# Kernel tuning notes

Measured on AMD Instinct MI355X. Metric: run time of the kernel, lower is better.

Reference implementation:

```python
import jax, jax.numpy as jnp
import numpy as np

N_LAYERS = 2

def setup_inputs() -> dict:
    key = jax.random.key(0)
    ks = jax.random.split(key, 11)
    B, T, S, H, V = 32, 64, 128, 1024, 32000
    dec_input = jax.random.randint(ks[0], (B, T), 0, V)
    h0 = jax.random.normal(ks[1], (N_LAYERS, B, H), jnp.float32)
    c0 = jax.random.normal(ks[2], (N_LAYERS, B, H), jnp.float32)
    encoder_outputs = jax.random.normal(ks[3], (B, S, H), jnp.float32)
    emb = jax.random.normal(ks[4], (V, H), jnp.float32) * 0.02
    emb = emb.at[0].set(0.0)  # padding_idx = 0
    W_ih = jax.random.normal(ks[5], (N_LAYERS, 4 * H, H), jnp.float32) * 0.02
    W_hh = jax.random.normal(ks[6], (N_LAYERS, 4 * H, H), jnp.float32) * 0.02
    b_ih = jax.random.normal(ks[7], (N_LAYERS, 4 * H), jnp.float32) * 0.02
    b_hh = jax.random.normal(ks[8], (N_LAYERS, 4 * H), jnp.float32) * 0.02
    cls_W = jax.random.normal(ks[9], (V, H), jnp.float32) * 0.02
    cls_b = jax.random.normal(ks[10], (V,), jnp.float32) * 0.02
    return dict(dec_input=dec_input, h0=h0, c0=c0, encoder_outputs=encoder_outputs,
                emb=emb, W_ih=W_ih, W_hh=W_hh, b_ih=b_ih, b_hh=b_hh,
                cls_W=cls_W, cls_b=cls_b)


def reference(dec_input, h0, c0, encoder_outputs, emb, W_ih, W_hh, b_ih, b_hh, cls_W, cls_b):
    # embedding (+dropout p=0) then relu, as in the torch forward
    x = jax.nn.relu(jnp.take(emb, dec_input, axis=0))  # [B,T,H]

    def step(carry, x_t):  # x_t: [B,H]
        h, c = carry  # each [L,B,H]
        inp = x_t
        new_h, new_c = [], []
        for i in range(N_LAYERS):
            gates = inp @ W_ih[i].T + b_ih[i] + h[i] @ W_hh[i].T + b_hh[i]  # [B,4H]
            ig, fg, gg, og = jnp.split(gates, 4, axis=-1)  # PyTorch LSTMCell gate order
            ci = jax.nn.sigmoid(fg) * c[i] + jax.nn.sigmoid(ig) * jnp.tanh(gg)
            hi = jax.nn.sigmoid(og) * jnp.tanh(ci)
            new_h.append(hi)
            new_c.append(ci)
            # residual (dims match since embedding_dim == rnn_dim)
            inp = hi + inp
        last = inp  # StackLSTMCell returns residual-accumulated output
        # dot attention: scores = context bmm target -> softmax (combine Linear output is discarded upstream)
        attn = jax.nn.softmax(jnp.einsum('bsh,bh->bs', encoder_outputs, last), axis=-1)
        return (jnp.stack(new_h), jnp.stack(new_c)), (last, attn)

    (hT, cT), (outs, attns) = jax.lax.scan(step, (h0, c0), jnp.swapaxes(x, 0, 1))
    outputs = jnp.swapaxes(outs, 0, 1)  # [B,T,H]
    logits = jnp.einsum('bth,vh->btv', outputs, cls_W) + cls_b  # [B,T,V]
    attn_scores = jnp.transpose(attns, (1, 2, 0))  # stack dim=2 -> [B,S,T]
    return logits, hT, cT, attn_scores
```

## Files before the change

### kernel.cpp

```cpp
#include <hip/hip_runtime.h>
#include <math.h>

typedef _Float16 f16x8 __attribute__((ext_vector_type(8)));
typedef _Float16 f16x4 __attribute__((ext_vector_type(4)));
typedef float    f32x4 __attribute__((ext_vector_type(4)));
typedef unsigned long long u64;
typedef unsigned int u32;

#define ALOAD(p)    __hip_atomic_load((p), __ATOMIC_RELAXED, __HIP_MEMORY_SCOPE_AGENT)
#define ASTORE(p,v) __hip_atomic_store((p), (v), __ATOMIC_RELAXED, __HIP_MEMORY_SCOPE_AGENT)

__global__ __launch_bounds__(256) void k_f32_to_f16(const float* __restrict__ src,
                                                    _Float16* __restrict__ dst, int n4) {
  int i = blockIdx.x * 256 + threadIdx.x;
  int stride = gridDim.x * 256;
  for (; i < n4; i += stride) {
    float4 v = ((const float4*)src)[i];
    f16x4 o;
    o.x = (_Float16)v.x; o.y = (_Float16)v.y; o.z = (_Float16)v.z; o.w = (_Float16)v.w;
    ((f16x4*)dst)[i] = o;
  }
}

__global__ __launch_bounds__(256) void k_pack0(const float* __restrict__ Whh0,
                                               _Float16* __restrict__ P) {
  int li = blockIdx.x * 256 + threadIdx.x;
  int row = li >> 7, k8 = li & 127;
  const float* s = Whh0 + (size_t)row * 1024 + k8 * 8;
  int g = row >> 10, u = row & 1023, jb = u >> 4, col = u & 15;
  int kh = k8 >> 4, rem = k8 & 15, st = rem >> 2, kslot = rem & 3;
  size_t idx = ((size_t)(((jb * 8 + kh) * 4 + st) * 4 + g)) * 64 + kslot * 16 + col;
  f16x8 o;
#pragma unroll
  for (int j = 0; j < 8; ++j) o[j] = (_Float16)s[j];
  *(f16x8*)(P + idx * 8) = o;
}

__global__ __launch_bounds__(256) void k_pack1(const float* __restrict__ Wih1,
                                               const float* __restrict__ Whh1,
                                               _Float16* __restrict__ P) {
  int li = blockIdx.x * 256 + threadIdx.x;
  int mat = li >> 19;
  int li2 = li & 524287;
  int row = li2 >> 7, k8l = li2 & 127;
  const float* s = (mat ? Whh1 : Wih1) + (size_t)row * 1024 + k8l * 8;
  int g = row >> 10, u = row & 1023, jb = u >> 4, col = u & 15;
  int k8g = mat * 128 + k8l;
  int kh = k8g >> 5, rem = k8g & 31, st = rem >> 2, kslot = rem & 3;
  size_t idx = ((size_t)(((jb * 8 + kh) * 8 + st) * 4 + g)) * 64 + kslot * 16 + col;
  f16x8 o;
#pragma unroll
  for (int j = 0; j < 8; ++j) o[j] = (_Float16)s[j];
  *(f16x8*)(P + idx * 8) = o;
}

__global__ __launch_bounds__(256) void k_embed(const int* __restrict__ dec,
                                               const float* __restrict__ emb,
                                               float* __restrict__ xf,
                                               _Float16* __restrict__ xh) {
  int i = blockIdx.x * 256 + threadIdx.x;
  int r = i >> 8;
  int c4 = i & 255;
  int b = r & 31, t = r >> 5;
  int tok = dec[b * 64 + t];
  float4 v = ((const float4*)(emb + (size_t)tok * 1024))[c4];
  v.x = fmaxf(v.x, 0.f); v.y = fmaxf(v.y, 0.f); v.z = fmaxf(v.z, 0.f); v.w = fmaxf(v.w, 0.f);
  ((float4*)(xf + (size_t)r * 1024))[c4] = v;
  f16x4 o;
  o.x = (_Float16)v.x; o.y = (_Float16)v.y; o.z = (_Float16)v.z; o.w = (_Float16)v.w;
  ((f16x4*)(xh + (size_t)r * 1024))[c4] = o;
}

__global__ __launch_bounds__(256) void k_init(const float* __restrict__ h0, const float* __restrict__ c0,
                                              float* __restrict__ c,
                                              _Float16* __restrict__ h0S, _Float16* __restrict__ h1S,
                                              int* __restrict__ bar) {
  int i = blockIdx.x * 256 + threadIdx.x;
  float hv = h0[i];
  c[i] = c0[i];
  if (i < 32768) h0S[i] = (_Float16)hv;
  else           h1S[i - 32768] = (_Float16)hv;
  if (i < 640) bar[i] = 0;
}

__global__ __launch_bounds__(256) void k_gemm0(const _Float16* __restrict__ A,
                                               const _Float16* __restrict__ Bm,
                                               const float* __restrict__ bias0,
                                               const float* __restrict__ bias1,
                                               float* __restrict__ C) {
  __shared__ _Float16 As[4 * 128 * 8];
  __shared__ _Float16 Bs[4 * 128 * 8];
  const int tid = threadIdx.x;
  const int lane = tid & 63;
  const int w = tid >> 6;
  const int wm = w >> 1, wn = w & 1;
  const _Float16* Ab = A + (size_t)blockIdx.y * 128 * 1024;
  const _Float16* Bb = Bm + (size_t)blockIdx.x * 128 * 1024;
  f32x4 acc[4][4] = {};
  for (int kc = 0; kc < 32; ++kc) {
#pragma unroll
    for (int ii = 0; ii < 2; ++ii) {
      int idx = tid + ii * 256;
      int kb = idx >> 7, row = idx & 127;
      int gofs = row * 1024 + kc * 32 + kb * 8;
      int sofs = kb * 1024 + row * 8;
      *(f16x8*)(As + sofs) = *(const f16x8*)(Ab + gofs);
      *(f16x8*)(Bs + sofs) = *(const f16x8*)(Bb + gofs);
    }
    __syncthreads();
    const int kb = lane >> 4;
    f16x8 af[4], bfv[4];
#pragma unroll
    for (int mf = 0; mf < 4; ++mf) {
      int row = wm * 64 + mf * 16 + (lane & 15);
      af[mf] = *(const f16x8*)(As + kb * 1024 + row * 8);
    }
#pragma unroll
    for (int nf = 0; nf < 4; ++nf) {
      int row = wn * 64 + nf * 16 + (lane & 15);
      bfv[nf] = *(const f16x8*)(Bs + kb * 1024 + row * 8);
    }
#pragma unroll
    for (int mf = 0; mf < 4; ++mf)
#pragma unroll
      for (int nf = 0; nf < 4; ++nf)
        acc[mf][nf] = __builtin_amdgcn_mfma_f32_16x16x32_f16(af[mf], bfv[nf], acc[mf][nf], 0, 0, 0);
    __syncthreads();
  }
  const int rl = (lane >> 4) * 4;
#pragma unroll
  for (int mf = 0; mf < 4; ++mf) {
#pragma unroll
    for (int nf = 0; nf < 4; ++nf) {
#pragma unroll
      for (int j = 0; j < 4; ++j) {
        int m = wm * 64 + mf * 16 + rl + j;
        int n = wn * 64 + nf * 16 + (lane & 15);
        int rg = blockIdx.y * 128 + m;
        int ng = blockIdx.x * 128 + n;
        C[(size_t)rg * 8192 + ng] = acc[mf][nf][j] + bias0[ng] + bias1[ng];
      }
    }
  }
}

__device__ __forceinline__ void gbar(int* bar) {
  __syncthreads();
  if (threadIdx.x == 0) {
    int* gen = bar + 544;
    int g = ALOAD(gen);
    int grp = blockIdx.x >> 3;
    int a = __hip_atomic_fetch_add(bar + grp * 32, 1, __ATOMIC_RELAXED, __HIP_MEMORY_SCOPE_AGENT);
    if (a == 7) {
      ASTORE(bar + grp * 32, 0);
      int r = __hip_atomic_fetch_add(bar + 512, 1, __ATOMIC_RELAXED, __HIP_MEMORY_SCOPE_AGENT);
      if (r == 15) {
        ASTORE(bar + 512, 0);
        ASTORE(gen, g + 1);
      }
    }
    while (ALOAD(gen) == g) __builtin_amdgcn_s_sleep(1);
  }
  __syncthreads();
}

template <int ROLE>
__device__ __forceinline__ void run_phases(
    int jb, const _Float16* __restrict__ Pk,
    const float* __restrict__ gx, const float* __restrict__ x_f,
    float* __restrict__ c_f,
    _Float16* __restrict__ h0S, _Float16* __restrict__ h1S,
    float* __restrict__ ipfA, float* __restrict__ ipfB,
    float* __restrict__ outs_f, _Float16* __restrict__ outs_h,
    float* __restrict__ outHT, float* __restrict__ outCT,
    int* bar, _Float16* As) {
  constexpr int S = ROLE ? 8 : 4;
  constexpr int NHALF = ROLE ? 2 : 1;
  constexpr int RSH = ROLE ? 8 : 7;
  constexpr int K8M = ROLE ? 255 : 127;
  const int u0 = jb * 16;
  const int tid = threadIdx.x;
  const int lane = tid & 63;
  const int kh = tid >> 6;
  const int col = lane & 15;
  const int kslot = lane >> 4;

  float* cst = c_f + ROLE * 32768;
  const float* gxbase = gx + (ROLE ? 4096 : 0);
  const int cb = tid >> 4, cul = tid & 15, cu = u0 + cul;

  const _Float16* pkbase = Pk + ((size_t)(jb * 8 + kh) * S) * 4 * 512 + lane * 8;
  const int a0off = col * 2056 + kh * S * 32 + kslot * 8;
  const int a1off = a0off + 16 * 2056;

  f16x8 wreg[S * 4];
#pragma unroll
  for (int i = 0; i < S * 4; ++i) wreg[i] = *(const f16x8*)(pkbase + i * 512);

  for (int p = 0; p <= 64; ++p) {
    const bool active = (ROLE == 0) ? (p < 64) : (p > 0);
    if (active) {
      const int t = (ROLE == 0) ? p : p - 1;
      const _Float16* h0r = h0S + (size_t)p * 32768;
      _Float16* h0w = h0S + (size_t)(p + 1) * 32768;
      const _Float16* h1r = h1S + (size_t)(p - 1) * 32768;
      _Float16* h1w = h1S + (size_t)p * 32768;
      const float* ipfr; float* ipfw;
      if (p & 1) { ipfr = ipfA; ipfw = ipfB; }
      else       { ipfr = ipfB; ipfw = ipfA; }

      const float* gxr = gxbase + (size_t)(t * 32 + cb) * 8192;
      float pg0 = gxr[cu], pg1 = gxr[1024 + cu], pg2 = gxr[2048 + cu], pg3 = gxr[3072 + cu];
      float pc = cst[cb * 1024 + cu];
      float px = 0.f, pip = 0.f;
      if (ROLE == 0) px = x_f[(size_t)(t * 32 + cb) * 1024 + cu];
      else           pip = ALOAD(ipfr + cb * 1024 + cu);

#pragma unroll
      for (int hf = 0; hf < NHALF; ++hf) {
        f16x8 sreg[8];
#pragma unroll
        for (int i = 0; i < 8; ++i) {
          int fr = (hf * 8 + i) * 512 + tid;
          int row = fr >> RSH, k8 = fr & K8M;
          const _Float16* s;
          if (ROLE == 0) s = h0r + row * 1024 + k8 * 8;
          else           s = (k8 < 128) ? (h0r + row * 1024 + k8 * 8)
                                        : (h1r + row * 1024 + (k8 - 128) * 8);
          sreg[i] = *(const f16x8*)s;
        }
#pragma unroll
        for (int i = 0; i < 8; ++i) {
          int fr = (hf * 8 + i) * 512 + tid;
          int row = fr >> RSH, k8 = fr & K8M;
          *(f16x8*)(As + row * 2056 + k8 * 8) = sreg[i];
        }
      }
      __syncthreads();

      f32x4 acc[2][4] = {};
#pragma unroll
      for (int s2 = 0; s2 < S; ++s2) {
        f16x8 a0 = *(const f16x8*)(As + a0off + s2 * 32);
        f16x8 a1 = *(const f16x8*)(As + a1off + s2 * 32);
        acc[0][0] = __builtin_amdgcn_mfma_f32_16x16x32_f16(a0, wreg[s2 * 4 + 0], acc[0][0], 0, 0, 0);
        acc[1][0] = __builtin_amdgcn_mfma_f32_16x16x32_f16(a1, wreg[s2 * 4 + 0], acc[1][0], 0, 0, 0);
        acc[0][1] = __builtin_amdgcn_mfma_f32_16x16x32_f16(a0, wreg[s2 * 4 + 1], acc[0][1], 0, 0, 0);
        acc[1][1] = __builtin_amdgcn_mfma_f32_16x16x32_f16(a1, wreg[s2 * 4 + 1], acc[1][1], 0, 0, 0);
        acc[0][2] = __builtin_amdgcn_mfma_f32_16x16x32_f16(a0, wreg[s2 * 4 + 2], acc[0][2], 0, 0, 0);
        acc[1][2] = __builtin_amdgcn_mfma_f32_16x16x32_f16(a1, wreg[s2 * 4 + 2], acc[1][2], 0, 0, 0);
        acc[0][3] = __builtin_amdgcn_mfma_f32_16x16x32_f16(a0, wreg[s2 * 4 + 3], acc[0][3], 0, 0, 0);
        acc[1][3] = __builtin_amdgcn_mfma_f32_16x16x32_f16(a1, wreg[s2 * 4 + 3], acc[1][3], 0, 0, 0);
      }
      __syncthreads();

      float (*gs)[32][68] = (float (*)[32][68])(void*)As;
      const int rl = kslot * 4;
      if (kh < 4) {
#pragma unroll
        for (int m = 0; m < 2; ++m)
#pragma unroll
          for (int g = 0; g < 4; ++g)
#pragma unroll
            for (int j = 0; j < 4; ++j)
              gs[kh][m * 16 + rl + j][g * 16 + col] = acc[m][g][j];
      }
      __syncthreads();
      if (kh >= 4) {
#pragma unroll
        for (int m = 0; m < 2; ++m)
#pragma unroll
          for (int g = 0; g < 4; ++g)
#pragma unroll
            for (int j = 0; j < 4; ++j)
              gs[kh - 4][m * 16 + rl + j][g * 16 + col] += acc[m][g][j];
      }
      __syncthreads();

      {
        float ig = pg0, fg = pg1, gg = pg2, og = pg3;
#pragma unroll
        for (int cc = 0; cc < 4; ++cc) {
          ig += gs[cc][cb][cul];
          fg += gs[cc][cb][16 + cul];
          gg += gs[cc][cb][32 + cul];
          og += gs[cc][cb][48 + cul];
        }
        float si = 1.f / (1.f + expf(-ig));
        float sf = 1.f / (1.f + expf(-fg));
        float so = 1.f / (1.f + expf(-og));
        float ci = sf * pc + si * tanhf(gg);
        float hi = so * tanhf(ci);
        cst[cb * 1024 + cu] = ci;
        if (t == 63) {
          outHT[ROLE * 32768 + cb * 1024 + cu] = hi;
          outCT[ROLE * 32768 + cb * 1024 + cu] = ci;
        }
        if (ROLE == 0) {
          float hn = __shfl_down(hi, 1);
          float ipv = hi + px;
          float ipn = __shfl_down(ipv, 1);
          if ((cul & 1) == 0) {
            union { _Float16 h[2]; u32 v; } ph;
            ph.h[0] = (_Float16)hi; ph.h[1] = (_Float16)hn;
            ASTORE((u32*)(h0w + cb * 1024 + cu), ph.v);
            union { float f[2]; u64 v; } pi;
            pi.f[0] = ipv; pi.f[1] = ipn;
            ASTORE((u64*)(ipfw + cb * 1024 + cu), pi.v);
          }
        } else {
          float hn = __shfl_down(hi, 1);
          float ro = hi + pip;
          float rn = __shfl_down(ro, 1);
          if ((cul & 1) == 0) {
            union { _Float16 h[2]; u32 v; } ph;
            ph.h[0] = (_Float16)hi; ph.h[1] = (_Float16)hn;
            ASTORE((u32*)(h1w + cb * 1024 + cu), ph.v);
            union { _Float16 h[2]; u32 v; } po;
            po.h[0] = (_Float16)ro; po.h[1] = (_Float16)rn;
            ASTORE((u32*)(outs_h + (size_t)(t * 32 + cb) * 1024 + cu), po.v);
          }
          outs_f[(size_t)(t * 32 + cb) * 1024 + cu] = ro;
        }
      }
    }
    gbar(bar);
  }
}

__device__ __forceinline__ void conv_clsW(const float* __restrict__ src,
                                          _Float16* __restrict__ dst, int cb) {
  for (int i = cb * 512 + threadIdx.x; i < 4096000; i += 65536) {
    const f32x4* s = (const f32x4*)(src + (size_t)i * 8);
    f32x4 v0 = __builtin_nontemporal_load(s);
    f32x4 v1 = __builtin_nontemporal_load(s + 1);
    union { _Float16 h[8]; u64 q[2]; } o;
    o.h[0] = (_Float16)v0.x; o.h[1] = (_Float16)v0.y;
    o.h[2] = (_Float16)v0.z; o.h[3] = (_Float16)v0.w;
    o.h[4] = (_Float16)v1.x; o.h[5] = (_Float16)v1.y;
    o.h[6] = (_Float16)v1.z; o.h[7] = (_Float16)v1.w;
    u64* d = (u64*)(dst + (size_t)i * 8);
    ASTORE(d, o.q[0]);
    ASTORE(d + 1, o.q[1]);
  }
}

__device__ __forceinline__ void run_consumer(
    const _Float16* __restrict__ outs_h, const _Float16* __restrict__ clsW_h,
    const float* __restrict__ cls_b, float* __restrict__ out, int* bar, _Float16* lds) {
  __shared__ int tau_s;
  const int tid = threadIdx.x;
  const int lane = tid & 63;
  const int w = tid >> 6;
  const int wm = w >> 2, wn = w & 3;
  int* gen = bar + 544;
  int* wcnt = bar + 576;
  const int r0 = tid & 255, kb0 = tid >> 8;

  if (tid == 0) {
    while (ALOAD(bar + 608) < 128) __builtin_amdgcn_s_sleep(16);
  }
  __syncthreads();

  for (;;) {
    if (tid == 0) tau_s = __hip_atomic_fetch_add(wcnt, 1, __ATOMIC_RELAXED, __HIP_MEMORY_SCOPE_AGENT);
    __syncthreads();
    int tau = tau_s;
    if (tau >= 1000) break;
    int m = tau / 125, nt = tau - m * 125;
    if (tid == 0) {
      int need = 8 * m + 9; if (need > 65) need = 65;
      while (ALOAD(gen) < need) __builtin_amdgcn_s_sleep(64);
    }
    __syncthreads();

    const _Float16* Ab = outs_h + (size_t)m * 256 * 1024;
    const _Float16* Bb = clsW_h + (size_t)nt * 256 * 1024;
    f16x8 pa0, pa1, pb0, pb1;
    pa0 = *(const f16x8*)(Ab + r0 * 1024 + kb0 * 8);
    pa1 = *(const f16x8*)(Ab + r0 * 1024 + (kb0 + 2) * 8);
    pb0 = *(const f16x8*)(Bb + r0 * 1024 + kb0 * 8);
    pb1 = *(const f16x8*)(Bb + r0 * 1024 + (kb0 + 2) * 8);
    f32x4 acc[8][4] = {};
    for (int kc = 0; kc < 32; ++kc) {
      _Float16* Ac = lds + (kc & 1) * 8192;
      _Float16* Bc = lds + 16384 + (kc & 1) * 8192;
      *(f16x8*)(Ac + kb0 * 2048 + r0 * 8) = pa0;
      *(f16x8*)(Ac + (kb0 + 2) * 2048 + r0 * 8) = pa1;
      *(f16x8*)(Bc + kb0 * 2048 + r0 * 8) = pb0;
      *(f16x8*)(Bc + (kb0 + 2) * 2048 + r0 * 8) = pb1;
      if (kc + 1 < 32) {
        int ko = (kc + 1) * 32;
        pa0 = *(const f16x8*)(Ab + r0 * 1024 + ko + kb0 * 8);
        pa1 = *(const f16x8*)(Ab + r0 * 1024 + ko + (kb0 + 2) * 8);
        pb0 = *(const f16x8*)(Bb + r0 * 1024 + ko + kb0 * 8);
        pb1 = *(const f16x8*)(Bb + r0 * 1024 + ko + (kb0 + 2) * 8);
      }
      __syncthreads();
      const int kb = lane >> 4;
      f16x8 af[8], bf[4];
#pragma unroll
      for (int mf = 0; mf < 8; ++mf) {
        int row = wm * 128 + mf * 16 + (lane & 15);
        af[mf] = *(const f16x8*)(Ac + kb * 2048 + row * 8);
      }
#pragma unroll
      for (int nf = 0; nf < 4; ++nf) {
        int row = wn * 64 + nf * 16 + (lane & 15);
        bf[nf] = *(const f16x8*)(Bc + kb * 2048 + row * 8);
      }
#pragma unroll
      for (int mf = 0; mf < 8; ++mf)
#pragma unroll
        for (int nf = 0; nf < 4; ++nf)
          acc[mf][nf] = __builtin_amdgcn_mfma_f32_16x16x32_f16(af[mf], bf[nf], acc[mf][nf], 0, 0, 0);
    }
    const int rl = (lane >> 4) * 4;
#pragma unroll
    for (int mf = 0; mf < 8; ++mf) {
#pragma unroll
      for (int nf = 0; nf < 4; ++nf) {
#pragma unroll
        for (int j = 0; j < 4; ++j) {
          int rg = m * 256 + wm * 128 + mf * 16 + rl + j;
          int tt = rg >> 5, b = rg & 31;
          int ng = nt * 256 + wn * 64 + nf * 16 + (lane & 15);
          __builtin_nontemporal_store(acc[mf][nf][j] + cls_b[ng],
                                      &out[(size_t)(b * 64 + tt) * 32000 + ng]);
        }
      }
    }
  }
}

__global__ __launch_bounds__(512, 1) void k_lstm_fused(
    const _Float16* __restrict__ Pk0, const _Float16* __restrict__ Pk1,
    const float* __restrict__ gx, const float* __restrict__ x_f,
    float* __restrict__ c_f,
    _Float16* __restrict__ h0S, _Float16* __restrict__ h1S,
    float* __restrict__ ipfA, float* __restrict__ ipfB,
    float* __restrict__ outs_f, _Float16* __restrict__ outs_h,
    const float* __restrict__ cls_W, _Float16* __restrict__ clsW_h,
    const float* __restrict__ cls_b,
    float* __restrict__ out_logits,
    float* __restrict__ outHT, float* __restrict__ outCT,
    int* bar) {
  __shared__ _Float16 As[32 * 2056];
  const int bid = blockIdx.x;
  if (bid < 64) {
    run_phases<0>(bid & 63, Pk0, gx, x_f, c_f, h0S, h1S,
                  ipfA, ipfB, outs_f, outs_h, outHT, outCT, bar, As);
  } else if (bid < 128) {
    run_phases<1>(bid & 63, Pk1, gx, x_f, c_f, h0S, h1S,
                  ipfA, ipfB, outs_f, outs_h, outHT, outCT, bar, As);
  } else {
    conv_clsW(cls_W, clsW_h, bid - 128);
    __syncthreads();
    if (threadIdx.x == 0)
      __hip_atomic_fetch_add(bar + 608, 1, __ATOMIC_RELAXED, __HIP_MEMORY_SCOPE_AGENT);
  }
  run_consumer(outs_h, clsW_h, cls_b, out_logits, bar, As);
}

__global__ __launch_bounds__(256) void k_attn(const float* __restrict__ outs,
                                              const float* __restrict__ enc,
                                              float* __restrict__ att) {
  __shared__ float o_s[8][1024];
  __shared__ float sc[8][128];
  const int tid = threadIdx.x;
  const int lane = tid & 63;
  const int w = tid >> 6;
  const int b = blockIdx.x >> 3;
  const int t0 = (blockIdx.x & 7) * 8;
#pragma unroll
  for (int ii = 0; ii < 8; ++ii) {
    int idx = tid + ii * 256;
    int tt = idx >> 8, c4 = idx & 255;
    ((float4*)&o_s[tt][0])[c4] =
        *(const float4*)(outs + (size_t)((t0 + tt) * 32 + b) * 1024 + (size_t)c4 * 4);
  }
  __syncthreads();
  for (int si = 0; si < 32; ++si) {
    int s = w * 32 + si;
    float av[8] = {0, 0, 0, 0, 0, 0, 0, 0};
    const float* er = enc + (size_t)(b * 128 + s) * 1024;
#pragma unroll
    for (int i = 0; i < 4; ++i) {
      int k = i * 256 + lane * 4;
      float4 e = *(const float4*)(er + k);
#pragma unroll
      for (int tt = 0; tt < 8; ++tt) {
        float4 o = *(const float4*)&o_s[tt][k];
        av[tt] += e.x * o.x + e.y * o.y + e.z * o.z + e.w * o.w;
      }
    }
#pragma unroll
    for (int tt = 0; tt < 8; ++tt) {
      float v = av[tt];
#pragma unroll
      for (int off = 32; off > 0; off >>= 1) v += __shfl_down(v, off);
      if (lane == 0) sc[tt][s] = v;
    }
  }
  __syncthreads();
#pragma unroll
  for (int pp = 0; pp < 2; ++pp) {
    int tt = w + pp * 4;
    float a = sc[tt][lane], b2 = sc[tt][64 + lane];
    float m = fmaxf(a, b2);
#pragma unroll
    for (int off = 32; off > 0; off >>= 1) m = fmaxf(m, __shfl_xor(m, off));
    float e0 = expf(a - m), e1 = expf(b2 - m);
    float ss = e0 + e1;
#pragma unroll
    for (int off = 32; off > 0; off >>= 1) ss += __shfl_xor(ss, off);
    float r = 1.f / ss;
    att[(size_t)b * 8192 + (size_t)lane * 64 + t0 + tt] = e0 * r;
    att[(size_t)b * 8192 + (size_t)(64 + lane) * 64 + t0 + tt] = e1 * r;
  }
}

extern "C" void kernel_launch(void* const* d_in, const int* in_sizes, int n_in,
                              void* d_out, int out_size, void* d_ws, size_t ws_size,
                              hipStream_t stream) {
  const int*   dec   = (const int*)d_in[0];
  const float* h0    = (const float*)d_in[1];
  const float* c0    = (const float*)d_in[2];
  const float* enc   = (const float*)d_in[3];
  const float* emb   = (const float*)d_in[4];
  const float* W_ih  = (const float*)d_in[5];
  const float* W_hh  = (const float*)d_in[6];
  const float* b_ih  = (const float*)d_in[7];
  const float* b_hh  = (const float*)d_in[8];
  const float* cls_W = (const float*)d_in[9];
  const float* cls_b = (const float*)d_in[10];
  float* out = (float*)d_out;
  char* ws = (char*)d_ws;

  float*    x_f    = (float*)(ws + 0);
  _Float16* x_h    = (_Float16*)(ws + 8388608);
  _Float16* Pk0    = (_Float16*)(ws + 8388608);
  _Float16* Wih_h  = (_Float16*)(ws + 12582912);
  _Float16* h0S    = (_Float16*)(ws + 16777216);
  _Float16* h1S    = (_Float16*)(ws + 21037056);
  _Float16* Pk1    = (_Float16*)(ws + 29360128);
  _Float16* clsW_h = (_Float16*)(ws + 46137344);
  float*    gx     = (float*)(ws + 111673344);
  float*    outs_f = (float*)(ws + 178782208);
  _Float16* outs_h = (_Float16*)(ws + 187170816);
  float*    c_f    = (float*)(ws + 191627264);
  int*      bar    = (int*)(ws + 192151552);
  float*    ipfA   = (float*)(ws + 192155648);
  float*    ipfB   = (float*)(ws + 192286720);

  k_f32_to_f16<<<2048, 256, 0, stream>>>(W_ih, Wih_h, 2097152);
  k_embed<<<2048, 256, 0, stream>>>(dec, emb, x_f, x_h);
  k_pack1<<<4096, 256, 0, stream>>>(W_ih + (size_t)4096 * 1024, W_hh + (size_t)4096 * 1024, Pk1);
  k_gemm0<<<dim3(64, 16), 256, 0, stream>>>(x_h, Wih_h, b_ih, b_hh, gx);
  k_pack0<<<2048, 256, 0, stream>>>(W_hh, Pk0);
  k_init<<<256, 256, 0, stream>>>(h0, c0, c_f, h0S, h1S, bar);

  k_lstm_fused<<<256, 512, 0, stream>>>(Pk0, Pk1, gx, x_f, c_f,
                                        h0S, h1S, ipfA, ipfB,
                                        outs_f, outs_h, cls_W, clsW_h, cls_b, out,
                                        out + (size_t)65536000, out + (size_t)65601536,
                                        bar);

  k_attn<<<256, 256, 0, stream>>>(outs_f, enc, out + (size_t)65667072);
}
```

Before: 699.5 us.

## Fuse preprocessing kernels into one launch and enlarge double-buffered input GEMM tile

Merges the f32-to-f16 conversion, embedding gather, weight packing and state init kernels into a single block-partitioned prep kernel, and moves the Wih_h and x_h buffers so Pk0 packing no longer aliases them. The layer-0 input-projection GEMM now uses 256x256 tiles with 512 threads, register prefetch and double-buffered LDS, with one barrier per k-step. This cuts launch overhead and gives more reuse per LDS load, at the cost of more registers per thread and fewer GEMM blocks (256).

```diff
diff --git a/kernel.cpp b/kernel.cpp
--- a/kernel.cpp
+++ b/kernel.cpp
@@ -10,134 +10,134 @@
 #define ALOAD(p)    __hip_atomic_load((p), __ATOMIC_RELAXED, __HIP_MEMORY_SCOPE_AGENT)
 #define ASTORE(p,v) __hip_atomic_store((p), (v), __ATOMIC_RELAXED, __HIP_MEMORY_SCOPE_AGENT)
 
-__global__ __launch_bounds__(256) void k_f32_to_f16(const float* __restrict__ src,
-                                                    _Float16* __restrict__ dst, int n4) {
-  int i = blockIdx.x * 256 + threadIdx.x;
-  int stride = gridDim.x * 256;
-  for (; i < n4; i += stride) {
-    float4 v = ((const float4*)src)[i];
+__global__ __launch_bounds__(256) void k_prep(
+    const float* __restrict__ W_ih, _Float16* __restrict__ Wih_h,
+    const int* __restrict__ dec, const float* __restrict__ emb,
+    float* __restrict__ xf, _Float16* __restrict__ xh,
+    const float* __restrict__ W_hh, _Float16* __restrict__ Pk0, _Float16* __restrict__ Pk1,
+    const float* __restrict__ h0, const float* __restrict__ c0,
+    float* __restrict__ c, _Float16* __restrict__ h0S, _Float16* __restrict__ h1S,
+    int* __restrict__ bar) {
+  const int bid = blockIdx.x;
+  const int tid = threadIdx.x;
+  if (bid < 2048) {
+#pragma unroll
+    for (int q = 0; q < 4; ++q) {
+      int i = q * 524288 + bid * 256 + tid;
+      float4 v = ((const float4*)W_ih)[i];
+      f16x4 o;
+      o.x = (_Float16)v.x; o.y = (_Float16)v.y; o.z = (_Float16)v.z; o.w = (_Float16)v.w;
+      ((f16x4*)Wih_h)[i] = o;
+    }
+  } else if (bid < 4096) {
+    int i = (bid - 2048) * 256 + tid;
+    int r = i >> 8, c4 = i & 255;
+    int b = r & 31, t = r >> 5;
+    int tok = dec[b * 64 + t];
+    float4 v = ((const float4*)(emb + (size_t)tok * 1024))[c4];
+    v.x = fmaxf(v.x, 0.f); v.y = fmaxf(v.y, 0.f); v.z = fmaxf(v.z, 0.f); v.w = fmaxf(v.w, 0.f);
+    ((float4*)(xf + (size_t)r * 1024))[c4] = v;
     f16x4 o;
     o.x = (_Float16)v.x; o.y = (_Float16)v.y; o.z = (_Float16)v.z; o.w = (_Float16)v.w;
-    ((f16x4*)dst)[i] = o;
-  }
-}
-
-__global__ __launch_bounds__(256) void k_pack0(const float* __restrict__ Whh0,
-                                               _Float16* __restrict__ P) {
-  int li = blockIdx.x * 256 + threadIdx.x;
-  int row = li >> 7, k8 = li & 127;
-  const float* s = Whh0 + (size_t)row * 1024 + k8 * 8;
-  int g = row >> 10, u = row & 1023, jb = u >> 4, col = u & 15;
-  int kh = k8 >> 4, rem = k8 & 15, st = rem >> 2, kslot = rem & 3;
-  size_t idx = ((size_t)(((jb * 8 + kh) * 4 + st) * 4 + g)) * 64 + kslot * 16 + col;
-  f16x8 o;
-#pragma unroll
-  for (int j = 0; j < 8; ++j) o[j] = (_Float16)s[j];
-  *(f16x8*)(P + idx * 8) = o;
-}
-
-__global__ __launch_bounds__(256) void k_pack1(const float* __restrict__ Wih1,
-                                               const float* __restrict__ Whh1,
-                                               _Float16* __restrict__ P) {
-  int li = blockIdx.x * 256 + threadIdx.x;
-  int mat = li >> 19;
-  int li2 = li & 524287;
-  int row = li2 >> 7, k8l = li2 & 127;
-  const float* s = (mat ? Whh1 : Wih1) + (size_t)row * 1024 + k8l * 8;
-  int g = row >> 10, u = row & 1023, jb = u >> 4, col = u & 15;
-  int k8g = mat * 128 + k8l;
-  int kh = k8g >> 5, rem = k8g & 31, st = rem >> 2, kslot = rem & 3;
-  size_t idx = ((size_t)(((jb * 8 + kh) * 8 + st) * 4 + g)) * 64 + kslot * 16 + col;
-  f16x8 o;
-#pragma unroll
-  for (int j = 0; j < 8; ++j) o[j] = (_Float16)s[j];
-  *(f16x8*)(P + idx * 8) = o;
-}
-
-__global__ __launch_bounds__(256) void k_embed(const int* __restrict__ dec,
-                                               const float* __restrict__ emb,
-                                               float* __restrict__ xf,
-                                               _Float16* __restrict__ xh) {
-  int i = blockIdx.x * 256 + threadIdx.x;
-  int r = i >> 8;
-  int c4 = i & 255;
-  int b = r & 31, t = r >> 5;
-  int tok = dec[b * 64 + t];
-  float4 v = ((const float4*)(emb + (size_t)tok * 1024))[c4];
-  v.x = fmaxf(v.x, 0.f); v.y = fmaxf(v.y, 0.f); v.z = fmaxf(v.z, 0.f); v.w = fmaxf(v.w, 0.f);
-  ((float4*)(xf + (size_t)r * 1024))[c4] = v;
-  f16x4 o;
-  o.x = (_Float16)v.x; o.y = (_Float16)v.y; o.z = (_Float16)v.z; o.w = (_Float16)v.w;
-  ((f16x4*)(xh + (size_t)r * 1024))[c4] = o;
-}
-
-__global__ __launch_bounds__(256) void k_init(const float* __restrict__ h0, const float* __restrict__ c0,
-                                              float* __restrict__ c,
-                                              _Float16* __restrict__ h0S, _Float16* __restrict__ h1S,
-                                              int* __restrict__ bar) {
-  int i = blockIdx.x * 256 + threadIdx.x;
-  float hv = h0[i];
-  c[i] = c0[i];
-  if (i < 32768) h0S[i] = (_Float16)hv;
-  else           h1S[i - 32768] = (_Float16)hv;
-  if (i < 640) bar[i] = 0;
-}
-
-__global__ __launch_bounds__(256) void k_gemm0(const _Float16* __restrict__ A,
-                                               const _Float16* __restrict__ Bm,
-                                               const float* __restrict__ bias0,
-                                               const float* __restrict__ bias1,
-                                               float* __restrict__ C) {
-  __shared__ _Float16 As[4 * 128 * 8];
-  __shared__ _Float16 Bs[4 * 128 * 8];
+    ((f16x4*)(xh + (size_t)r * 1024))[c4] = o;
+  } else if (bid < 8192) {
+    int li = (bid - 4096) * 256 + tid;
+    int mat = li >> 19;
+    int li2 = li & 524287;
+    int row = li2 >> 7, k8l = li2 & 127;
+    const float* s = (mat ? (W_hh + (size_t)4096 * 1024) : (W_ih + (size_t)4096 * 1024))
+                     + (size_t)row * 1024 + k8l * 8;
+    int g = row >> 10, u = row & 1023, jb = u >> 4, col = u & 15;
+    int k8g = mat * 128 + k8l;
+    int kh = k8g >> 5, rem = k8g & 31, st = rem >> 2, kslot = rem & 3;
+    size_t idx = ((size_t)(((jb * 8 + kh) * 8 + st) * 4 + g)) * 64 + kslot * 16 + col;
+    f16x8 o;
+#pragma unroll
+    for (int j = 0; j < 8; ++j) o[j] = (_Float16)s[j];
+    *(f16x8*)(Pk1 + idx * 8) = o;
+  } else if (bid < 10240) {
+    int li = (bid - 8192) * 256 + tid;
+    int row = li >> 7, k8 = li & 127;
+    const float* s = W_hh + (size_t)row * 1024 + k8 * 8;
+    int g = row >> 10, u = row & 1023, jb = u >> 4, col = u & 15;
+    int kh = k8 >> 4, rem = k8 & 15, st = rem >> 2, kslot = rem & 3;
+    size_t idx = ((size_t)(((jb * 8 + kh) * 4 + st) * 4 + g)) * 64 + kslot * 16 + col;
+    f16x8 o;
+#pragma unroll
+    for (int j = 0; j < 8; ++j) o[j] = (_Float16)s[j];
+    *(f16x8*)(Pk0 + idx * 8) = o;
+  } else {
+    int i = (bid - 10240) * 256 + tid;
+    float hv = h0[i];
+    c[i] = c0[i];
+    if (i < 32768) h0S[i] = (_Float16)hv;
+    else           h1S[i - 32768] = (_Float16)hv;
+    if (i < 640) bar[i] = 0;
+  }
+}
+
+__global__ __launch_bounds__(512) void k_gemm0b(const _Float16* __restrict__ A,
+                                                const _Float16* __restrict__ Bm,
+                                                const float* __restrict__ bias0,
+                                                const float* __restrict__ bias1,
+                                                float* __restrict__ C) {
+  __shared__ _Float16 lds2[32768];
   const int tid = threadIdx.x;
   const int lane = tid & 63;
   const int w = tid >> 6;
-  const int wm = w >> 1, wn = w & 1;
-  const _Float16* Ab = A + (size_t)blockIdx.y * 128 * 1024;
-  const _Float16* Bb = Bm + (size_t)blockIdx.x * 128 * 1024;
-  f32x4 acc[4][4] = {};
+  const int wm = w >> 2, wn = w & 3;
+  const int r0 = tid & 255, kb0 = tid >> 8;
+  const int m = blockIdx.y, nt = blockIdx.x;
+  const _Float16* Ab = A + (size_t)m * 256 * 1024;
+  const _Float16* Bb = Bm + (size_t)nt * 256 * 1024;
+  f16x8 pa0, pa1, pb0, pb1;
+  pa0 = *(const f16x8*)(Ab + r0 * 1024 + kb0 * 8);
+  pa1 = *(const f16x8*)(Ab + r0 * 1024 + (kb0 + 2) * 8);
+  pb0 = *(const f16x8*)(Bb + r0 * 1024 + kb0 * 8);
+  pb1 = *(const f16x8*)(Bb + r0 * 1024 + (kb0 + 2) * 8);
+  f32x4 acc[8][4] = {};
   for (int kc = 0; kc < 32; ++kc) {
-#pragma unroll
-    for (int ii = 0; ii < 2; ++ii) {
-      int idx = tid + ii * 256;
-      int kb = idx >> 7, row = idx & 127;
-      int gofs = row * 1024 + kc * 32 + kb * 8;
-      int sofs = kb * 1024 + row * 8;
-      *(f16x8*)(As + sofs) = *(const f16x8*)(Ab + gofs);
-      *(f16x8*)(Bs + sofs) = *(const f16x8*)(Bb + gofs);
+    _Float16* Ac = lds2 + (kc & 1) * 8192;
+    _Float16* Bc = lds2 + 16384 + (kc & 1) * 8192;
+    *(f16x8*)(Ac + kb0 * 2048 + r0 * 8) = pa0;
+    *(f16x8*)(Ac + (kb0 + 2) * 2048 + r0 * 8) = pa1;
+    *(f16x8*)(Bc + kb0 * 2048 + r0 * 8) = pb0;
+    *(f16x8*)(Bc + (kb0 + 2) * 2048 + r0 * 8) = pb1;
+    if (kc + 1 < 32) {
+      int ko = (kc + 1) * 32;
+      pa0 = *(const f16x8*)(Ab + r0 * 1024 + ko + kb0 * 8);
+      pa1 = *(const f16x8*)(Ab + r0 * 1024 + ko + (kb0 + 2) * 8);
+      pb0 = *(const f16x8*)(Bb + r0 * 1024 + ko + kb0 * 8);
+      pb1 = *(const f16x8*)(Bb + r0 * 1024 + ko + (kb0 + 2) * 8);
     }
     __syncthreads();
     const int kb = lane >> 4;
-    f16x8 af[4], bfv[4];
-#pragma unroll
-    for (int mf = 0; mf < 4; ++mf) {
-      int row = wm * 64 + mf * 16 + (lane & 15);
-      af[mf] = *(const f16x8*)(As + kb * 1024 + row * 8);
+    f16x8 af[8], bf[4];
+#pragma unroll
+    for (int mf = 0; mf < 8; ++mf) {
+      int row = wm * 128 + mf * 16 + (lane & 15);
+      af[mf] = *(const f16x8*)(Ac + kb * 2048 + row * 8);
     }
 #pragma unroll
     for (int nf = 0; nf < 4; ++nf) {
       int row = wn * 64 + nf * 16 + (lane & 15);
-      bfv[nf] = *(const f16x8*)(Bs + kb * 1024 + row * 8);
-    }
-#pragma unroll
-    for (int mf = 0; mf < 4; ++mf)
+      bf[nf] = *(const f16x8*)(Bc + kb * 2048 + row * 8);
+    }
+#pragma unroll
+    for (int mf = 0; mf < 8; ++mf)
 #pragma unroll
       for (int nf = 0; nf < 4; ++nf)
-        acc[mf][nf] = __builtin_amdgcn_mfma_f32_16x16x32_f16(af[mf], bfv[nf], acc[mf][nf], 0, 0, 0);
-    __syncthreads();
+        acc[mf][nf] = __builtin_amdgcn_mfma_f32_16x16x32_f16(af[mf], bf[nf], acc[mf][nf], 0, 0, 0);
   }
   const int rl = (lane >> 4) * 4;
 #pragma unroll
-  for (int mf = 0; mf < 4; ++mf) {
+  for (int mf = 0; mf < 8; ++mf) {
 #pragma unroll
     for (int nf = 0; nf < 4; ++nf) {
 #pragma unroll
       for (int j = 0; j < 4; ++j) {
-        int m = wm * 64 + mf * 16 + rl + j;
-        int n = wn * 64 + nf * 16 + (lane & 15);
-        int rg = blockIdx.y * 128 + m;
-        int ng = blockIdx.x * 128 + n;
+        int rg = m * 256 + wm * 128 + mf * 16 + rl + j;
+        int ng = nt * 256 + wn * 64 + nf * 16 + (lane & 15);
         C[(size_t)rg * 8192 + ng] = acc[mf][nf][j] + bias0[ng] + bias1[ng];
       }
     }
@@ -538,13 +538,13 @@
   char* ws = (char*)d_ws;
 
   float*    x_f    = (float*)(ws + 0);
-  _Float16* x_h    = (_Float16*)(ws + 8388608);
   _Float16* Pk0    = (_Float16*)(ws + 8388608);
-  _Float16* Wih_h  = (_Float16*)(ws + 12582912);
   _Float16* h0S    = (_Float16*)(ws + 16777216);
   _Float16* h1S    = (_Float16*)(ws + 21037056);
   _Float16* Pk1    = (_Float16*)(ws + 29360128);
   _Float16* clsW_h = (_Float16*)(ws + 46137344);
+  _Float16* Wih_h  = (_Float16*)(ws + 54657024);
+  _Float16* x_h    = (_Float16*)(ws + 71434240);
   float*    gx     = (float*)(ws + 111673344);
   float*    outs_f = (float*)(ws + 178782208);
   _Float16* outs_h = (_Float16*)(ws + 187170816);
@@ -553,12 +553,9 @@
   float*    ipfA   = (float*)(ws + 192155648);
   float*    ipfB   = (float*)(ws + 192286720);
 
-  k_f32_to_f16<<<2048, 256, 0, stream>>>(W_ih, Wih_h, 2097152);
-  k_embed<<<2048, 256, 0, stream>>>(dec, emb, x_f, x_h);
-  k_pack1<<<4096, 256, 0, stream>>>(W_ih + (size_t)4096 * 1024, W_hh + (size_t)4096 * 1024, Pk1);
-  k_gemm0<<<dim3(64, 16), 256, 0, stream>>>(x_h, Wih_h, b_ih, b_hh, gx);
-  k_pack0<<<2048, 256, 0, stream>>>(W_hh, Pk0);
-  k_init<<<256, 256, 0, stream>>>(h0, c0, c_f, h0S, h1S, bar);
+  k_prep<<<10496, 256, 0, stream>>>(W_ih, Wih_h, dec, emb, x_f, x_h,
+                                    W_hh, Pk0, Pk1, h0, c0, c_f, h0S, h1S, bar);
+  k_gemm0b<<<dim3(32, 8), 512, 0, stream>>>(x_h, Wih_h, b_ih, b_hh, gx);
 
   k_lstm_fused<<<256, 512, 0, stream>>>(Pk0, Pk1, gx, x_f, c_f,
                                         h0S, h1S, ipfA, ipfB,
```

Result: faster. 666.2 us, median of 2 (-4.8%).
